# Performance work log

Measured on AMD Instinct MI355X. Metric: run time of the kernel, lower is better.

The kernel has to match this reference:

```python
import jax, jax.numpy as jnp
import numpy as np

D_MODEL = 1024
N_HEADS = 16
HEAD_DIM = D_MODEL // N_HEADS
B, T = 4, 2048


def setup_inputs() -> dict:
    key = jax.random.key(0)
    k1, k2, k3, k4 = jax.random.split(key, 4)
    x = jax.random.normal(k1, (B, T, D_MODEL), dtype=jnp.float32)
    # bool key-padding mask: True = masked (padded) position
    pad_mask = jax.random.randint(k2, (B, T), 0, 2).astype(jnp.bool_)
    # torch Linear weights: [out_features, in_features], bias=False
    W_qkv = jax.random.normal(k3, (3 * D_MODEL, D_MODEL), dtype=jnp.float32) * (1.0 / np.sqrt(D_MODEL))
    W_proj = jax.random.normal(k4, (D_MODEL, D_MODEL), dtype=jnp.float32) * (1.0 / np.sqrt(D_MODEL))
    return {"x": x, "pad_mask": pad_mask, "W_qkv": W_qkv, "W_proj": W_proj}


def reference(x, pad_mask, W_qkv, W_proj):
    Bv, Tv, C = x.shape
    H, Dh = N_HEADS, HEAD_DIM
    # qkv projection: x @ W_qkv.T -> [B,T,3C], reshape to [B,T,3,H,Dh]
    qkv = jnp.einsum('btc,oc->bto', x, W_qkv).reshape(Bv, Tv, 3, H, Dh)
    q = jnp.transpose(qkv[:, :, 0], (0, 2, 1, 3))  # [B,H,T,Dh]
    k = jnp.transpose(qkv[:, :, 1], (0, 2, 1, 3))
    v = jnp.transpose(qkv[:, :, 2], (0, 2, 1, 3))
    scale = 1.0 / jnp.sqrt(jnp.asarray(Dh, x.dtype))
    attn = jnp.einsum('bhqd,bhkd->bhqk', q, k) * scale  # [B,H,T,T]
    # key-padding mask: broadcast [B,1,1,T]
    attn = jnp.where(pad_mask[:, None, None, :], -jnp.inf, attn)
    attn = jax.nn.softmax(attn, axis=-1)
    out = jnp.einsum('bhqk,bhkd->bhqd', attn, v)  # [B,H,T,Dh]
    out = jnp.transpose(out, (0, 2, 1, 3)).reshape(Bv, Tv, C)
    return jnp.einsum('btc,oc->bto', out, W_proj)
```

## Files before the change

### kernel.cpp

```cpp
#include <hip/hip_runtime.h>
#include <hip/hip_bf16.h>
#include <stdint.h>

typedef __bf16 bf16_t;
typedef __bf16 bf16x8 __attribute__((ext_vector_type(8)));
typedef __bf16 bf16x4 __attribute__((ext_vector_type(4)));
typedef float f32x4 __attribute__((ext_vector_type(4)));

#define DEVFN static __device__ __forceinline__

DEVFN f32x4 mfma16(bf16x8 a, bf16x8 b, f32x4 c) {
  return __builtin_amdgcn_mfma_f32_16x16x32_bf16(a, b, c, 0, 0, 0);
}

#define GLL16(gsrc, ldst) __builtin_amdgcn_global_load_lds( \
    (__attribute__((address_space(1))) void*)(gsrc), \
    (__attribute__((address_space(3))) void*)(ldst), 16, 0, 0)

#define SCALE_Q 0.1803368801111204f

__global__ void cvt_all(const float* __restrict__ x, const float* __restrict__ wqkv,
                        const float* __restrict__ wproj, bf16_t* __restrict__ xb,
                        bf16_t* __restrict__ wqkvb, bf16_t* __restrict__ wprojb) {
  const int i = blockIdx.x * 256 + threadIdx.x;
  const float* s;
  bf16_t* d;
  int off;
  if (i < 2097152) { s = x; d = xb; off = i; }
  else if (i < 2097152 + 786432) { s = wqkv; d = wqkvb; off = i - 2097152; }
  else { s = wproj; d = wprojb; off = i - 2883584; }
  f32x4 v = reinterpret_cast<const f32x4*>(s)[off];
  bf16x4 o;
  o[0] = (bf16_t)v[0]; o[1] = (bf16_t)v[1]; o[2] = (bf16_t)v[2]; o[3] = (bf16_t)v[3];
  reinterpret_cast<bf16x4*>(d)[off] = o;
}

__global__ void build_idx(const int* __restrict__ mask, int* __restrict__ tc,
                          int* __restrict__ nk, bf16_t* __restrict__ kb,
                          bf16_t* __restrict__ vtb) {
  const int b = blockIdx.x;
  const int tid = threadIdx.x;
  const int lane = tid & 63, wv = tid >> 6;
  __shared__ int nk_s;
  const int* mrow = mask + b * 2048;
  if (wv == 0) {
    int base = 0;
    for (int cs = 0; cs < 2048; cs += 64) {
      const int mval = mrow[cs + lane];
      const unsigned long long bal = __ballot(mval == 0);
      const int pre = __popcll(bal & ((1ull << lane) - 1ull));
      if (!mval) tc[b * 2048 + base + pre] = cs + lane;
      base += __popcll(bal);
    }
    if (lane == 0) nk_s = base;
  }
  __syncthreads();
  const int nkb = nk_s;
  if (tid == 0) nk[b] = nkb;
  for (int i = nkb + tid; i < 2048; i += 256) tc[b * 2048 + i] = -1;
  const int ce = (nkb + 63) & ~63;
  for (int hh = wv; hh < 16; hh += 4) {
    const size_t bh = (size_t)(b * 16 + hh);
    for (int r = nkb; r < ce; ++r) {
      kb[(bh * 2048 + r) * 64 + lane] = (bf16_t)0.f;
      vtb[(bh * 64 + lane) * 2048 + r] = (bf16_t)0.f;
    }
  }
}

template <int EPI>
__global__ __launch_bounds__(256, 2)
void gemm_ct(const bf16_t* __restrict__ A, const bf16_t* __restrict__ Bx,
             bf16_t* __restrict__ qb, bf16_t* __restrict__ kb,
             bf16_t* __restrict__ vtb, float* __restrict__ fout,
             const int* __restrict__ tc, const int* __restrict__ nkp) {
  constexpr int K = 1024;
  __shared__ alignas(16) unsigned short At[128 * 64];
  __shared__ alignas(16) unsigned short Bt[128 * 64];
  const int tid = threadIdx.x;
  const int lane = tid & 63, w = tid >> 6;
  const int c = lane & 15, g = lane >> 4;
  const int bid = blockIdx.x;
  const int xcd = bid & 7, jj = bid >> 3;
  const int my = xcd * 8 + (jj & 7);
  const int bx = jj >> 3;
  const int oBase = bx * 128, mBase = my * 128;
  const int wo = (w >> 1) * 64, wm = (w & 1) * 64;

  int nkb = 0;
  bool kv = false;
  if (EPI == 0) {
    nkb = nkp[mBase >> 11];
    kv = (bx >= 8);
    if (kv && (mBase & 2047) >= nkb) return;
  }
  int brow[4];
#pragma unroll
  for (int i = 0; i < 4; ++i) {
    const int r = (i * 4 + w) * 8 + (lane >> 3);
    if (EPI == 0 && kv) {
      const int t = tc[(mBase >> 11) * 2048 + (mBase & 2047) + r];
      brow[i] = (mBase & ~2047) + (t < 0 ? 0 : t);
    } else {
      brow[i] = mBase + r;
    }
  }

  f32x4 acc[4][4] = {};

  for (int k0 = 0; k0 < K; k0 += 64) {
#pragma unroll
    for (int i = 0; i < 4; ++i) {
      const int cid = (i * 4 + w) * 64 + lane;
      const int r = cid >> 3;
      const int ss = (cid & 7) ^ (r & 7);
      GLL16(A + (size_t)(oBase + r) * K + k0 + ss * 8, &At[(i * 4 + w) * 512]);
      GLL16(Bx + (size_t)brow[i] * K + k0 + ss * 8, &Bt[(i * 4 + w) * 512]);
    }
    __syncthreads();
    bf16x8 af[4][2], bfr[4][2];
#pragma unroll
    for (int f = 0; f < 4; ++f) {
#pragma unroll
      for (int kc = 0; kc < 2; ++kc) {
        const int ra = wo + f * 16 + c;
        af[f][kc] = *reinterpret_cast<const bf16x8*>(&At[ra * 64 + ((kc * 4 + g) ^ (ra & 7)) * 8]);
        const int rb = wm + f * 16 + c;
        bfr[f][kc] = *reinterpret_cast<const bf16x8*>(&Bt[rb * 64 + ((kc * 4 + g) ^ (rb & 7)) * 8]);
      }
    }
    __builtin_amdgcn_s_setprio(1);
#pragma unroll
    for (int of = 0; of < 4; ++of)
#pragma unroll
      for (int mf = 0; mf < 4; ++mf)
#pragma unroll
        for (int kc = 0; kc < 2; ++kc)
          acc[of][mf] = mfma16(af[of][kc], bfr[mf][kc], acc[of][mf]);
    __builtin_amdgcn_s_setprio(0);
    __syncthreads();
  }

#pragma unroll
  for (int of = 0; of < 4; ++of) {
    const int o0 = oBase + wo + of * 16 + g * 4;
#pragma unroll
    for (int mf = 0; mf < 4; ++mf) {
      const int m = mBase + wm + mf * 16 + c;
      f32x4 v = acc[of][mf];
      if (EPI == 0) {
        if (!kv) {
          v[0] *= SCALE_Q; v[1] *= SCALE_Q; v[2] *= SCALE_Q; v[3] *= SCALE_Q;
          bf16x4 bv;
          bv[0] = (bf16_t)v[0]; bv[1] = (bf16_t)v[1]; bv[2] = (bf16_t)v[2]; bv[3] = (bf16_t)v[3];
          const int rem = o0 & 1023;
          const int h = rem >> 6, d0 = rem & 63;
          const int b = m >> 11, t = m & 2047;
          *reinterpret_cast<bf16x4*>(qb + (((size_t)(b * 16 + h)) * 2048 + t) * 64 + d0) = bv;
        } else {
          const int i = m & 2047;
          if (i < nkb) {
            bf16x4 bv;
            bv[0] = (bf16_t)v[0]; bv[1] = (bf16_t)v[1]; bv[2] = (bf16_t)v[2]; bv[3] = (bf16_t)v[3];
            const int rem = o0 & 1023;
            const int h = rem >> 6, d0 = rem & 63;
            const int b = m >> 11;
            const size_t bh = (size_t)(b * 16 + h);
            if (bx < 16) {
              *reinterpret_cast<bf16x4*>(kb + (bh * 2048 + i) * 64 + d0) = bv;
            } else {
#pragma unroll
              for (int j = 0; j < 4; ++j)
                vtb[(bh * 64 + d0 + j) * 2048 + i] = bv[j];
            }
          }
        }
      } else {
        *reinterpret_cast<f32x4*>(fout + (size_t)m * 1024 + o0) = v;
      }
    }
  }
}

__global__ __launch_bounds__(256, 2)
void attn_fwd(const bf16_t* __restrict__ Qg, const bf16_t* __restrict__ Kg,
              const bf16_t* __restrict__ Vtg, const int* __restrict__ nkp,
              bf16_t* __restrict__ aout) {
  constexpr int T = 2048;
  __shared__ alignas(16) unsigned short KtL[2][64 * 64];
  __shared__ alignas(16) unsigned short VtL[2][64 * 64];
  const int tid = threadIdx.x, lane = tid & 63, w = tid >> 6;
  const int c = lane & 15, g = lane >> 4;
  const int bid = blockIdx.x;
  const int xcd = bid & 7, jj = bid >> 3;
  const int bh = xcd * 8 + (jj & 7), qp = jj >> 3;
  const int b = bh >> 4, h = bh & 15;
  const bf16_t* Qh = Qg + (size_t)bh * T * 64;
  const bf16_t* Kh = Kg + (size_t)bh * T * 64;
  const bf16_t* Vh = Vtg + (size_t)bh * 64 * T;
  const int q0 = qp * 256 + w * 64;
  const int nkb = nkp[b];
  const int ntiles = (nkb + 63) >> 6;

  bf16x8 qfr[4][2];
#pragma unroll
  for (int qq = 0; qq < 4; ++qq)
#pragma unroll
    for (int dc = 0; dc < 2; ++dc)
      qfr[qq][dc] = *reinterpret_cast<const bf16x8*>(
          Qh + (size_t)(q0 + qq * 16 + c) * 64 + dc * 32 + g * 8);

  bf16x8 ones;
#pragma unroll
  for (int i = 0; i < 8; ++i) ones[i] = (bf16_t)1.0f;

  f32x4 oacc[4][4] = {};
  float lrun[4] = {0.f, 0.f, 0.f, 0.f};

  auto stage = [&](int t, int bi) {
    const int kt0 = t * 64;
#pragma unroll
    for (int i = 0; i < 2; ++i) {
      const int cid = (i * 4 + w) * 64 + lane;
      const int r = cid >> 3, p = cid & 7;
      const int lk = p ^ ((r & 3) | (((r >> 3) & 1) << 2));
      GLL16(Kh + (size_t)(kt0 + r) * 64 + lk * 8, &KtL[bi][(i * 4 + w) * 512]);
      const int lv = p ^ (r & 7);
      GLL16(Vh + (size_t)r * T + kt0 + lv * 8, &VtL[bi][(i * 4 + w) * 512]);
    }
  };

  stage(0, 0);
  __syncthreads();

  const int fK = (c & 3) | (((c >> 2) & 1) << 2);

  for (int t = 0; t < ntiles; ++t) {
    const int cur = t & 1;
    if (t + 1 < ntiles) stage(t + 1, cur ^ 1);

    bf16x8 kfr[4][2];
#pragma unroll
    for (int kr = 0; kr < 4; ++kr) {
      const int row = (c >> 2) * 8 + (kr & 1) * 4 + (c & 3) + (kr >> 1) * 32;
#pragma unroll
      for (int dc = 0; dc < 2; ++dc)
        kfr[kr][dc] = *reinterpret_cast<const bf16x8*>(
            &KtL[cur][row * 64 + (((dc * 4 + g) ^ fK) * 8)]);
    }

    const bool tail = (t == ntiles - 1) && (nkb & 63) != 0;
    f32x4 bias4[4];
#pragma unroll
    for (int kr = 0; kr < 4; ++kr) {
      if (tail) {
        const int kbase = t * 64 + g * 8 + (kr & 1) * 4 + (kr >> 1) * 32;
#pragma unroll
        for (int j = 0; j < 4; ++j) bias4[kr][j] = (kbase + j < nkb) ? 0.f : -1e30f;
      } else {
        bias4[kr][0] = bias4[kr][1] = bias4[kr][2] = bias4[kr][3] = 0.f;
      }
    }

    bf16x8 pfr[4][2];
#pragma unroll
    for (int qq = 0; qq < 4; ++qq) {
      f32x4 stq[4];
      __builtin_amdgcn_s_setprio(1);
#pragma unroll
      for (int kr = 0; kr < 4; ++kr) {
        f32x4 z = mfma16(kfr[kr][0], qfr[qq][0], bias4[kr]);
        stq[kr] = mfma16(kfr[kr][1], qfr[qq][1], z);
      }
      __builtin_amdgcn_s_setprio(0);
#pragma unroll
      for (int kc = 0; kc < 2; ++kc) {
        bf16x8 p;
#pragma unroll
        for (int j = 0; j < 4; ++j) {
          p[j]     = (bf16_t)__builtin_amdgcn_exp2f(stq[kc * 2 + 0][j]);
          p[4 + j] = (bf16_t)__builtin_amdgcn_exp2f(stq[kc * 2 + 1][j]);
        }
        pfr[qq][kc] = p;
      }
      f32x4 su = {0.f, 0.f, 0.f, 0.f};
      su = mfma16(ones, pfr[qq][0], su);
      su = mfma16(ones, pfr[qq][1], su);
      lrun[qq] += su[0];
    }

    __builtin_amdgcn_s_setprio(1);
#pragma unroll
    for (int df = 0; df < 4; ++df) {
      bf16x8 va[2];
#pragma unroll
      for (int kc = 0; kc < 2; ++kc) {
        const int r = df * 16 + c;
        va[kc] = *reinterpret_cast<const bf16x8*>(
            &VtL[cur][r * 64 + ((kc * 4 + g) ^ (r & 7)) * 8]);
      }
#pragma unroll
      for (int qq = 0; qq < 4; ++qq)
#pragma unroll
        for (int kc = 0; kc < 2; ++kc)
          oacc[df][qq] = mfma16(va[kc], pfr[qq][kc], oacc[df][qq]);
    }
    __builtin_amdgcn_s_setprio(0);
    __syncthreads();
  }

#pragma unroll
  for (int qq = 0; qq < 4; ++qq) {
    const float inv = 1.0f / lrun[qq];
    const int q = q0 + qq * 16 + c;
#pragma unroll
    for (int df = 0; df < 4; ++df) {
      bf16x4 bv;
#pragma unroll
      for (int j = 0; j < 4; ++j) bv[j] = (bf16_t)(oacc[df][qq][j] * inv);
      const int d0 = df * 16 + g * 4;
      *reinterpret_cast<bf16x4*>(aout + ((size_t)(b * 2048 + q)) * 1024 + h * 64 + d0) = bv;
    }
  }
}

extern "C" void kernel_launch(void* const* d_in, const int* in_sizes, int n_in,
                              void* d_out, int out_size, void* d_ws, size_t ws_size,
                              hipStream_t stream) {
  (void)in_sizes; (void)n_in; (void)out_size; (void)ws_size;
  const float* x = (const float*)d_in[0];
  const int* pmask = (const int*)d_in[1];
  const float* wqkv = (const float*)d_in[2];
  const float* wproj = (const float*)d_in[3];
  float* out = (float*)d_out;
  char* ws = (char*)d_ws;

  bf16_t* xb    = (bf16_t*)(ws + 0);
  bf16_t* aob   = (bf16_t*)(ws + 0);
  bf16_t* wqkvb = (bf16_t*)(ws + 16777216);
  bf16_t* wprojb= (bf16_t*)(ws + 23068672);
  bf16_t* Qb    = (bf16_t*)(ws + 25165824);
  bf16_t* Kb    = (bf16_t*)(ws + 41943040);
  bf16_t* Vtb   = (bf16_t*)(ws + 58720256);

  int* tc  = (int*)d_out;
  int* nkp = tc + 4 * 2048;

  cvt_all<<<12288, 256, 0, stream>>>(x, wqkv, wproj, xb, wqkvb, wprojb);
  build_idx<<<4, 256, 0, stream>>>(pmask, tc, nkp, Kb, Vtb);

  gemm_ct<0><<<1536, 256, 0, stream>>>(wqkvb, xb, Qb, Kb, Vtb, nullptr, tc, nkp);
  attn_fwd<<<512, 256, 0, stream>>>(Qb, Kb, Vtb, nkp, aob);
  gemm_ct<1><<<512, 256, 0, stream>>>(wprojb, aob, nullptr, nullptr, nullptr, out,
                                      nullptr, nullptr);
}
```

Measured before the change: 151.1 us.

## Fuse conversion and mask-index kernels; use plain 2D grid for GEMMs

Merges the fp32-to-bf16 conversion kernel and the padding-index build kernel into one launch, removing one kernel launch and its gap. It also replaces the XCD-aware swizzled 1D block mapping in the GEMMs with a simple 2D grid (blockIdx.x over output columns, blockIdx.y over rows). The remapping changes which tiles share an XCD's L2, which may lose the locality the swizzle provided.

```diff
diff --git a/kernel.cpp b/kernel.cpp
--- a/kernel.cpp
+++ b/kernel.cpp
@@ -19,27 +19,28 @@
 
 #define SCALE_Q 0.1803368801111204f
 
-__global__ void cvt_all(const float* __restrict__ x, const float* __restrict__ wqkv,
-                        const float* __restrict__ wproj, bf16_t* __restrict__ xb,
-                        bf16_t* __restrict__ wqkvb, bf16_t* __restrict__ wprojb) {
-  const int i = blockIdx.x * 256 + threadIdx.x;
-  const float* s;
-  bf16_t* d;
-  int off;
-  if (i < 2097152) { s = x; d = xb; off = i; }
-  else if (i < 2097152 + 786432) { s = wqkv; d = wqkvb; off = i - 2097152; }
-  else { s = wproj; d = wprojb; off = i - 2883584; }
-  f32x4 v = reinterpret_cast<const f32x4*>(s)[off];
-  bf16x4 o;
-  o[0] = (bf16_t)v[0]; o[1] = (bf16_t)v[1]; o[2] = (bf16_t)v[2]; o[3] = (bf16_t)v[3];
-  reinterpret_cast<bf16x4*>(d)[off] = o;
-}
-
-__global__ void build_idx(const int* __restrict__ mask, int* __restrict__ tc,
-                          int* __restrict__ nk, bf16_t* __restrict__ kb,
-                          bf16_t* __restrict__ vtb) {
-  const int b = blockIdx.x;
+__global__ void prep(const float* __restrict__ x, const float* __restrict__ wqkv,
+                     const float* __restrict__ wproj, bf16_t* __restrict__ xb,
+                     bf16_t* __restrict__ wqkvb, bf16_t* __restrict__ wprojb,
+                     const int* __restrict__ mask, int* __restrict__ tc,
+                     int* __restrict__ nk, bf16_t* __restrict__ kb,
+                     bf16_t* __restrict__ vtb) {
   const int tid = threadIdx.x;
+  if (blockIdx.x < 12288) {
+    const int i = blockIdx.x * 256 + tid;
+    const float* s;
+    bf16_t* d;
+    int off;
+    if (i < 2097152) { s = x; d = xb; off = i; }
+    else if (i < 2097152 + 786432) { s = wqkv; d = wqkvb; off = i - 2097152; }
+    else { s = wproj; d = wprojb; off = i - 2883584; }
+    f32x4 v = reinterpret_cast<const f32x4*>(s)[off];
+    bf16x4 o;
+    o[0] = (bf16_t)v[0]; o[1] = (bf16_t)v[1]; o[2] = (bf16_t)v[2]; o[3] = (bf16_t)v[3];
+    reinterpret_cast<bf16x4*>(d)[off] = o;
+    return;
+  }
+  const int b = blockIdx.x - 12288;
   const int lane = tid & 63, wv = tid >> 6;
   __shared__ int nk_s;
   const int* mrow = mask + b * 2048;
@@ -80,18 +81,14 @@
   const int tid = threadIdx.x;
   const int lane = tid & 63, w = tid >> 6;
   const int c = lane & 15, g = lane >> 4;
-  const int bid = blockIdx.x;
-  const int xcd = bid & 7, jj = bid >> 3;
-  const int my = xcd * 8 + (jj & 7);
-  const int bx = jj >> 3;
-  const int oBase = bx * 128, mBase = my * 128;
+  const int oBase = blockIdx.x * 128, mBase = blockIdx.y * 128;
   const int wo = (w >> 1) * 64, wm = (w & 1) * 64;
 
   int nkb = 0;
   bool kv = false;
   if (EPI == 0) {
     nkb = nkp[mBase >> 11];
-    kv = (bx >= 8);
+    kv = (blockIdx.x >= 8);
     if (kv && (mBase & 2047) >= nkb) return;
   }
   int brow[4];
@@ -166,7 +163,7 @@
             const int h = rem >> 6, d0 = rem & 63;
             const int b = m >> 11;
             const size_t bh = (size_t)(b * 16 + h);
-            if (bx < 16) {
+            if (blockIdx.x < 16) {
               *reinterpret_cast<bf16x4*>(kb + (bh * 2048 + i) * 64 + d0) = bv;
             } else {
 #pragma unroll
@@ -346,11 +343,11 @@
   int* tc  = (int*)d_out;
   int* nkp = tc + 4 * 2048;
 
-  cvt_all<<<12288, 256, 0, stream>>>(x, wqkv, wproj, xb, wqkvb, wprojb);
-  build_idx<<<4, 256, 0, stream>>>(pmask, tc, nkp, Kb, Vtb);
-
-  gemm_ct<0><<<1536, 256, 0, stream>>>(wqkvb, xb, Qb, Kb, Vtb, nullptr, tc, nkp);
+  prep<<<12292, 256, 0, stream>>>(x, wqkv, wproj, xb, wqkvb, wprojb,
+                                  pmask, tc, nkp, Kb, Vtb);
+
+  gemm_ct<0><<<dim3(24, 64), 256, 0, stream>>>(wqkvb, xb, Qb, Kb, Vtb, nullptr, tc, nkp);
   attn_fwd<<<512, 256, 0, stream>>>(Qb, Kb, Vtb, nkp, aob);
-  gemm_ct<1><<<512, 256, 0, stream>>>(wprojb, aob, nullptr, nullptr, nullptr, out,
-                                      nullptr, nullptr);
-}
+  gemm_ct<1><<<dim3(8, 64), 256, 0, stream>>>(wprojb, aob, nullptr, nullptr, nullptr, out,
+                                              nullptr, nullptr);
+}
```

New measurement: 156.3 us, median of 3. 3.5% more time.
